# Kernel optimization log

Measured on AMD Instinct MI355X. Metric: run time of the kernel, lower is better.

Reference implementation:

```python
import jax, jax.numpy as jnp
import numpy as np

B, L, F = 4096, 128, 64
NODE_MAX = 1024  # padding id is 0


def setup_inputs() -> dict:
    key = jax.random.key(0)
    k1, k2, k3, k4, k5, k6 = jax.random.split(key, 6)
    src_ids = jax.random.randint(k1, (B, L), 0, NODE_MAX, dtype=jnp.int64)
    dst_ids = jax.random.randint(k2, (B, L), 0, NODE_MAX, dtype=jnp.int64)
    W1 = jax.random.normal(k3, (1, F), dtype=jnp.float32)
    b1 = jax.random.normal(k4, (F,), dtype=jnp.float32)
    W2 = jax.random.normal(k5, (F, F), dtype=jnp.float32) / jnp.sqrt(F)
    b2 = jax.random.normal(k6, (F,), dtype=jnp.float32)
    return {"src_ids": src_ids, "dst_ids": dst_ids, "W1": W1, "b1": b1, "W2": W2, "b2": b2}


def _pair_counts(a, b):
    """For each element of a[bi, i]: (count of that id in a's row, count in b's row).

    Equality-based counting is exactly equivalent to np.unique counts + dict lookup
    (missing ids simply match nothing -> count 0).
    """
    self_cnt = (a[:, :, None] == a[:, None, :]).astype(jnp.float32).sum(-1)   # [B,L]
    cross_cnt = (a[:, :, None] == b[:, None, :]).astype(jnp.float32).sum(-1)  # [B,L]
    return self_cnt, cross_cnt


def _encode(freq, W1, b1, W2, b2):
    # freq: [B,L,2] -> unsqueeze to [B,L,2,1] -> MLP -> sum over the 2-axis -> [B,L,F]
    h = jax.nn.relu(freq[..., None] * W1[0] + b1)          # [B,L,2,F]
    out = jnp.einsum("blcf,fg->blcg", h, W2) + b2          # [B,L,2,F]
    return out.sum(axis=2)                                  # [B,L,F]


def reference(src_ids, dst_ids, W1, b1, W2, b2):
    src_self, src_cross = _pair_counts(src_ids, dst_ids)
    dst_self, dst_cross = _pair_counts(dst_ids, src_ids)
    src_mask = (src_ids != 0).astype(jnp.float32)[..., None]  # zero padded positions
    dst_mask = (dst_ids != 0).astype(jnp.float32)[..., None]
    # source rows: [freq in src, freq in dst]; dst rows: [freq in dst, freq in src]
    src_freq = jnp.stack([src_self, src_cross], axis=-1) * src_mask  # [B,L,2]
    dst_freq = jnp.stack([dst_self, dst_cross], axis=-1) * dst_mask  # [B,L,2]
    src_feat = _encode(src_freq, W1, b1, W2, b2)
    dst_feat = _encode(dst_freq, W1, b1, W2, b2)
    return src_feat, dst_feat
```

## Files before the change

kernel.cpp:

```cpp
#include <hip/hip_runtime.h>

#define LDIM 128
#define FDIM 64
#define NVALS 129
#define NODE_MAX 1024

typedef float f32x4 __attribute__((ext_vector_type(4)));

__global__ __launch_bounds__(256) void build_table_kernel(
    const float* __restrict__ W1, const float* __restrict__ b1,
    const float* __restrict__ W2, const float* __restrict__ b2,
    float* __restrict__ T)
{
    const int t  = threadIdx.x;
    const int vi = t >> 6, g = t & 63;
    const int v  = blockIdx.x * 4 + vi;

    __shared__ float h[4][FDIM];
    h[vi][g] = fmaxf((float)v * W1[g] + b1[g], 0.0f);
    __syncthreads();

    if (v < NVALS) {
        float acc = b2[g];
#pragma unroll
        for (int f = 0; f < FDIM; ++f)
            acc = fmaf(h[vi][f], W2[f * FDIM + g], acc);
        T[v * FDIM + g] = acc;
    }
}

__global__ __launch_bounds__(256) void encode_rows_kernel(
    const int* __restrict__ src, const int* __restrict__ dst,
    const float* __restrict__ T,
    float* __restrict__ out_src, float* __restrict__ out_dst)
{
    const int b = blockIdx.x;
    const int t = threadIdx.x;

    __shared__ int sID[LDIM], dID[LDIM];
    __shared__ int histS[NODE_MAX], histD[NODE_MAX];
    __shared__ int aS[LDIM], bS[LDIM], aD[LDIM], bD[LDIM];

    ((int4*)histS)[t] = make_int4(0, 0, 0, 0);
    ((int4*)histD)[t] = make_int4(0, 0, 0, 0);
    if (t < LDIM) sID[t] = src[(size_t)b * LDIM + t];
    else          dID[t - LDIM] = dst[(size_t)b * LDIM + (t - LDIM)];
    __syncthreads();

    if (t < LDIM) atomicAdd(&histS[sID[t]], 1);
    else          atomicAdd(&histD[dID[t - LDIM]], 1);
    __syncthreads();

    if (t < LDIM) {
        const int id = sID[t];
        int a = histS[id], c = histD[id];
        if (id == 0) { a = 0; c = 0; }
        aS[t] = a; bS[t] = c;
    } else {
        const int id = dID[t - LDIM];
        int a = histD[id], c = histS[id];
        if (id == 0) { a = 0; c = 0; }
        aD[t - LDIM] = a; bD[t - LDIM] = c;
    }
    __syncthreads();

    const f32x4* __restrict__ T4 = (const f32x4*)T;
    f32x4* __restrict__ o4s = (f32x4*)out_src;
    f32x4* __restrict__ o4d = (f32x4*)out_dst;
    const size_t rowBase = (size_t)b * (LDIM * FDIM / 4);

#pragma unroll
    for (int k = 0; k < 8; ++k) {
        const int c   = t + k * 256;
        const int pos = c >> 4;
        const int ch  = c & 15;
        o4s[rowBase + c] = T4[aS[pos] * 16 + ch] + T4[bS[pos] * 16 + ch];
        o4d[rowBase + c] = T4[aD[pos] * 16 + ch] + T4[bD[pos] * 16 + ch];
    }
}

extern "C" void kernel_launch(void* const* d_in, const int* in_sizes, int n_in,
                              void* d_out, int out_size, void* d_ws, size_t ws_size,
                              hipStream_t stream)
{
    const int*   src = (const int*)d_in[0];
    const int*   dst = (const int*)d_in[1];
    const float* W1  = (const float*)d_in[2];
    const float* b1  = (const float*)d_in[3];
    const float* W2  = (const float*)d_in[4];
    const float* b2  = (const float*)d_in[5];

    float* out = (float*)d_out;
    float* T   = (float*)d_ws;

    const int B = in_sizes[0] / LDIM;
    const size_t half = (size_t)B * LDIM * FDIM;

    build_table_kernel<<<33, 256, 0, stream>>>(W1, b1, W2, b2, T);
    encode_rows_kernel<<<B, 256, 0, stream>>>(src, dst, T, out, out + half);
}
```

Baseline: 54.00 us.

## Stage lookup table in shared memory reusing histogram space

The encode kernel now copies the 129x64 float lookup table (about 33 KB) into shared memory, reusing the buffer that first holds the src/dst histograms. Output gathers then read the table from LDS instead of global memory or L2. The two count values per position are packed into one int, and the id loads are kept in registers. The price is about 33 KB of LDS per block, which may cap occupancy, plus a table copy and an extra barrier in every block.

New measurement: 55.28 us. +2.4%, slower.

```diff
diff --git a/kernel.cpp b/kernel.cpp
--- a/kernel.cpp
+++ b/kernel.cpp
@@ -4,6 +4,8 @@
 #define FDIM 64
 #define NVALS 129
 #define NODE_MAX 1024
+#define TBYTES (NVALS * FDIM * 4)
+#define TV4    (NVALS * FDIM / 4)
 
 typedef float f32x4 __attribute__((ext_vector_type(4)));
 
@@ -37,34 +39,41 @@
     const int b = blockIdx.x;
     const int t = threadIdx.x;
 
-    __shared__ int sID[LDIM], dID[LDIM];
-    __shared__ int histS[NODE_MAX], histD[NODE_MAX];
-    __shared__ int aS[LDIM], bS[LDIM], aD[LDIM], bD[LDIM];
+    __shared__ __align__(16) char tbl[TBYTES];
+    __shared__ int ids[2 * LDIM];
+    __shared__ int cnt[2 * LDIM];
 
-    ((int4*)histS)[t] = make_int4(0, 0, 0, 0);
-    ((int4*)histD)[t] = make_int4(0, 0, 0, 0);
-    if (t < LDIM) sID[t] = src[(size_t)b * LDIM + t];
-    else          dID[t - LDIM] = dst[(size_t)b * LDIM + (t - LDIM)];
+    int* hist = (int*)tbl;
+
+    const int myId = (t < LDIM) ? src[(size_t)b * LDIM + t]
+                                : dst[(size_t)b * LDIM + (t - LDIM)];
+    ((int4*)hist)[t]       = make_int4(0, 0, 0, 0);
+    ((int4*)hist)[t + 256] = make_int4(0, 0, 0, 0);
+    ids[t] = myId;
     __syncthreads();
 
-    if (t < LDIM) atomicAdd(&histS[sID[t]], 1);
-    else          atomicAdd(&histD[dID[t - LDIM]], 1);
+    atomicAdd(&hist[((t >> 7) << 10) + myId], 1);
     __syncthreads();
 
-    if (t < LDIM) {
-        const int id = sID[t];
-        int a = histS[id], c = histD[id];
-        if (id == 0) { a = 0; c = 0; }
-        aS[t] = a; bS[t] = c;
-    } else {
-        const int id = dID[t - LDIM];
-        int a = histD[id], c = histS[id];
-        if (id == 0) { a = 0; c = 0; }
-        aD[t - LDIM] = a; bD[t - LDIM] = c;
+    {
+        const int self_base  = (t >> 7) << 10;
+        const int cross_base = 1024 - self_base;
+        int a = hist[self_base + myId];
+        int c = hist[cross_base + myId];
+        if (myId == 0) { a = 0; c = 0; }
+        cnt[t] = a | (c << 8);
     }
     __syncthreads();
 
-    const f32x4* __restrict__ T4 = (const f32x4*)T;
+    {
+        f32x4*       dstv = (f32x4*)tbl;
+        const f32x4* srcv = (const f32x4*)T;
+        for (int i = t; i < TV4; i += 256)
+            dstv[i] = srcv[i];
+    }
+    __syncthreads();
+
+    const f32x4* __restrict__ T4 = (const f32x4*)tbl;
     f32x4* __restrict__ o4s = (f32x4*)out_src;
     f32x4* __restrict__ o4d = (f32x4*)out_dst;
     const size_t rowBase = (size_t)b * (LDIM * FDIM / 4);
@@ -74,8 +83,12 @@
         const int c   = t + k * 256;
         const int pos = c >> 4;
         const int ch  = c & 15;
-        o4s[rowBase + c] = T4[aS[pos] * 16 + ch] + T4[bS[pos] * 16 + ch];
-        o4d[rowBase + c] = T4[aD[pos] * 16 + ch] + T4[bD[pos] * 16 + ch];
+
+        const int qs = cnt[pos];
+        o4s[rowBase + c] = T4[(qs & 255) * 16 + ch] + T4[(qs >> 8) * 16 + ch];
+
+        const int qd = cnt[LDIM + pos];
+        o4d[rowBase + c] = T4[(qd & 255) * 16 + ch] + T4[(qd >> 8) * 16 + ch];
     }
 }
 
```
